# Kernel tuning notes

Hardware: AMD Instinct MI355X
Metric: run time of the kernel (lower is better)

The kernel has to match this reference:

```python
import jax, jax.numpy as jnp
import numpy as np

UFOLDS = 12
EPS = 1e-08


def _synapse_act(v, mu, sigma, W):
    # v: [B, P]; mu, sigma, W: [P, U] -> activation [B, P, U]
    g = jax.nn.sigmoid(sigma * (v[:, :, None] - mu))
    return W * g


def setup_inputs() -> dict:
    key = jax.random.key(0)
    ks = jax.random.split(key, 13)
    B, IN, U = 2048, 128, 256
    inputs = jax.random.normal(ks[0], (B, IN), dtype=jnp.float32)
    state = jax.random.normal(ks[1], (B, U), dtype=jnp.float32)
    # sensory synapse params (input_size, num_units)
    sensory_mu = jax.random.uniform(ks[2], (IN, U), minval=0.3, maxval=0.8)
    sensory_sigma = jax.random.uniform(ks[3], (IN, U), minval=3.0, maxval=8.0)
    sensory_W = jax.random.uniform(ks[4], (IN, U), minval=0.01, maxval=1.0)
    sensory_erev = jnp.sign(jax.random.normal(ks[5], (IN, U))).astype(jnp.float32)
    # recurrent synapse params (num_units, num_units)
    mu = jax.random.uniform(ks[6], (U, U), minval=0.3, maxval=0.8)
    sigma = jax.random.uniform(ks[7], (U, U), minval=3.0, maxval=8.0)
    W = jax.random.uniform(ks[8], (U, U), minval=0.01, maxval=1.0)
    erev = jnp.sign(jax.random.normal(ks[9], (U, U))).astype(jnp.float32)
    # leak / membrane params (num_units,)
    vleak = jax.random.uniform(ks[10], (U,), minval=-0.2, maxval=0.2)
    gleak = jnp.ones((U,), dtype=jnp.float32)          # gleak_init_min == gleak_init_max == 1
    cm_t = jnp.full((U,), 0.5, dtype=jnp.float32)      # cm_init_min == cm_init_max == 0.5
    return dict(inputs=inputs, state=state,
                sensory_mu=sensory_mu, sensory_sigma=sensory_sigma,
                sensory_W=sensory_W, sensory_erev=sensory_erev,
                mu=mu, sigma=sigma, W=W, erev=erev,
                vleak=vleak, gleak=gleak, cm_t=cm_t)


def reference(inputs, state, sensory_mu, sensory_sigma, sensory_W, sensory_erev,
              mu, sigma, W, erev, vleak, gleak, cm_t):
    # sensory path computed once, outside the fold loop
    s_act = _synapse_act(inputs, sensory_mu, sensory_sigma, sensory_W)  # [B, IN, U]
    w_den_sensory = jnp.sum(s_act, axis=1)                              # [B, U]
    w_num_sensory = jnp.sum(s_act * sensory_erev, axis=1)               # [B, U]

    gl_vl = gleak * vleak  # [U]

    def fold(v_pre, _):
        act = _synapse_act(v_pre, mu, sigma, W)           # [B, U, U]
        w_red = jnp.sum(act, axis=1)                       # [B, U]
        w_num = jnp.sum(act * erev, axis=1) + w_num_sensory
        numerator = cm_t * v_pre + gl_vl + w_num
        denominator = cm_t + gleak + w_red + w_den_sensory
        return numerator / (denominator + EPS), None

    v, _ = jax.lax.scan(fold, state, None, length=UFOLDS)
    return v
```

## Files before the change

kernel.cpp:

```cpp
#include <hip/hip_runtime.h>

#define NFOLDS 12
#define EPS 1e-8f
#define BATCH 2048
#define IN_DIM 128
#define UNITS 256
#define RB 4
#define LOG2E 1.44269504088896340736f

#if __has_builtin(__builtin_amdgcn_exp2f)
#define EXP2F(x) __builtin_amdgcn_exp2f(x)
#else
#define EXP2F(x) exp2f(x)
#endif

#if __has_builtin(__builtin_amdgcn_rcpf)
#define RCPF(x) __builtin_amdgcn_rcpf(x)
#else
#define RCPF(x) (1.0f / (x))
#endif

__global__ void prep_kernel(const float* __restrict__ mu,
                            const float* __restrict__ sigma,
                            const float* __restrict__ W,
                            const float* __restrict__ erev,
                            float4* __restrict__ out, int n) {
    int i = blockIdx.x * blockDim.x + threadIdx.x;
    if (i < n) {
        float A = sigma[i] * LOG2E;
        float w = W[i];
        out[i] = make_float4(-A, A * mu[i], w, w * erev[i]);
    }
}

__global__ __launch_bounds__(256, 2) void ltc_kernel(
    const float4* __restrict__ rp,
    const float4* __restrict__ sp,
    const float* __restrict__ inputs,
    const float* __restrict__ state,
    const float* __restrict__ vleak,
    const float* __restrict__ gleak,
    const float* __restrict__ cm_t,
    float* __restrict__ out)
{
    const int u = threadIdx.x;
    const int b0 = blockIdx.x * RB;

    __shared__ __align__(16) float v_sh[RB][UNITS];
    __shared__ float in_sh[RB][IN_DIM];

    #pragma unroll
    for (int rb = 0; rb < RB; ++rb)
        v_sh[rb][u] = state[(b0 + rb) * UNITS + u];
    #pragma unroll
    for (int k = u; k < RB * IN_DIM; k += UNITS) {
        int rb = k >> 7;
        int i  = k & (IN_DIM - 1);
        in_sh[rb][i] = inputs[(b0 + rb) * IN_DIM + i];
    }
    __syncthreads();

    float sden[RB], snum[RB];
    #pragma unroll
    for (int rb = 0; rb < RB; ++rb) { sden[rb] = 0.f; snum[rb] = 0.f; }

    for (int i = 0; i < IN_DIM; ++i) {
        float4 p = sp[i * UNITS + u];
        #pragma unroll
        for (int rb = 0; rb < RB; ++rb) {
            float t = fmaf(p.x, in_sh[rb][i], p.y);
            float e = EXP2F(t);
            float g = RCPF(1.0f + e);
            sden[rb] = fmaf(p.z, g, sden[rb]);
            snum[rb] = fmaf(p.w, g, snum[rb]);
        }
    }

    const float gl = gleak[u];
    const float cm = cm_t[u];
    const float glvl = gl * vleak[u];
    float den_base[RB], num_base[RB];
    #pragma unroll
    for (int rb = 0; rb < RB; ++rb) {
        den_base[rb] = cm + gl + sden[rb] + EPS;
        num_base[rb] = glvl + snum[rb];
    }

    float vnew[RB];
    for (int f = 0; f < NFOLDS; ++f) {
        float wred[RB], wnum[RB];
        #pragma unroll
        for (int rb = 0; rb < RB; ++rb) { wred[rb] = 0.f; wnum[rb] = 0.f; }

        for (int j = 0; j < UNITS; j += 4) {
            float4 p0 = rp[(j + 0) * UNITS + u];
            float4 p1 = rp[(j + 1) * UNITS + u];
            float4 p2 = rp[(j + 2) * UNITS + u];
            float4 p3 = rp[(j + 3) * UNITS + u];
            #pragma unroll
            for (int rb = 0; rb < RB; ++rb) {
                float4 v4 = *reinterpret_cast<const float4*>(&v_sh[rb][j]);
                {
                    float t = fmaf(p0.x, v4.x, p0.y);
                    float g = RCPF(1.0f + EXP2F(t));
                    wred[rb] = fmaf(p0.z, g, wred[rb]);
                    wnum[rb] = fmaf(p0.w, g, wnum[rb]);
                }
                {
                    float t = fmaf(p1.x, v4.y, p1.y);
                    float g = RCPF(1.0f + EXP2F(t));
                    wred[rb] = fmaf(p1.z, g, wred[rb]);
                    wnum[rb] = fmaf(p1.w, g, wnum[rb]);
                }
                {
                    float t = fmaf(p2.x, v4.z, p2.y);
                    float g = RCPF(1.0f + EXP2F(t));
                    wred[rb] = fmaf(p2.z, g, wred[rb]);
                    wnum[rb] = fmaf(p2.w, g, wnum[rb]);
                }
                {
                    float t = fmaf(p3.x, v4.w, p3.y);
                    float g = RCPF(1.0f + EXP2F(t));
                    wred[rb] = fmaf(p3.z, g, wred[rb]);
                    wnum[rb] = fmaf(p3.w, g, wnum[rb]);
                }
            }
        }

        #pragma unroll
        for (int rb = 0; rb < RB; ++rb) {
            float vp = v_sh[rb][u];
            float num = fmaf(cm, vp, num_base[rb]) + wnum[rb];
            float den = den_base[rb] + wred[rb];
            vnew[rb] = num / den;
        }
        __syncthreads();
        #pragma unroll
        for (int rb = 0; rb < RB; ++rb)
            v_sh[rb][u] = vnew[rb];
        __syncthreads();
    }

    #pragma unroll
    for (int rb = 0; rb < RB; ++rb)
        out[(b0 + rb) * UNITS + u] = vnew[rb];
}

extern "C" void kernel_launch(void* const* d_in, const int* in_sizes, int n_in,
                              void* d_out, int out_size, void* d_ws, size_t ws_size,
                              hipStream_t stream) {
    const float* inputs       = (const float*)d_in[0];
    const float* state        = (const float*)d_in[1];
    const float* sensory_mu   = (const float*)d_in[2];
    const float* sensory_sig  = (const float*)d_in[3];
    const float* sensory_W    = (const float*)d_in[4];
    const float* sensory_erev = (const float*)d_in[5];
    const float* mu           = (const float*)d_in[6];
    const float* sigma        = (const float*)d_in[7];
    const float* W            = (const float*)d_in[8];
    const float* erev         = (const float*)d_in[9];
    const float* vleak        = (const float*)d_in[10];
    const float* gleak        = (const float*)d_in[11];
    const float* cm_t         = (const float*)d_in[12];
    float* out = (float*)d_out;

    float4* rp = (float4*)d_ws;
    float4* sp = rp + UNITS * UNITS;

    int n_rec = UNITS * UNITS;
    int n_sen = IN_DIM * UNITS;
    prep_kernel<<<(n_rec + 255) / 256, 256, 0, stream>>>(mu, sigma, W, erev, rp, n_rec);
    prep_kernel<<<(n_sen + 255) / 256, 256, 0, stream>>>(sensory_mu, sensory_sig,
                                                         sensory_W, sensory_erev, sp, n_sen);

    ltc_kernel<<<BATCH / RB, UNITS, 0, stream>>>(rp, sp, inputs, state,
                                                 vleak, gleak, cm_t, out);
}
```

Before: 408.8 us.

## Split synapse reduction across two thread halves with shared-memory partial sums

Blocks grow from 256 to 512 threads. Each half sums over half of the presynaptic units (and half of the inputs in the sensory path), then the halves combine partial sums through shared memory. The goal is more waves per block and more latency hiding for the exp/rcp-heavy loop. The cost is an extra barrier per fold plus more shared-memory traffic, and the sensory loop now reads its inputs as vectorized float4.

```diff
diff --git a/kernel.cpp b/kernel.cpp
--- a/kernel.cpp
+++ b/kernel.cpp
@@ -33,7 +33,36 @@
     }
 }
 
-__global__ __launch_bounds__(256, 2) void ltc_kernel(
+__device__ __forceinline__ void syn4(const float4 p0, const float4 p1,
+                                     const float4 p2, const float4 p3,
+                                     const float4 v4, float& red, float& num) {
+    {
+        float t = fmaf(p0.x, v4.x, p0.y);
+        float g = RCPF(1.0f + EXP2F(t));
+        red = fmaf(p0.z, g, red);
+        num = fmaf(p0.w, g, num);
+    }
+    {
+        float t = fmaf(p1.x, v4.y, p1.y);
+        float g = RCPF(1.0f + EXP2F(t));
+        red = fmaf(p1.z, g, red);
+        num = fmaf(p1.w, g, num);
+    }
+    {
+        float t = fmaf(p2.x, v4.z, p2.y);
+        float g = RCPF(1.0f + EXP2F(t));
+        red = fmaf(p2.z, g, red);
+        num = fmaf(p2.w, g, num);
+    }
+    {
+        float t = fmaf(p3.x, v4.w, p3.y);
+        float g = RCPF(1.0f + EXP2F(t));
+        red = fmaf(p3.z, g, red);
+        num = fmaf(p3.w, g, num);
+    }
+}
+
+__global__ __launch_bounds__(512, 4) void ltc_kernel(
     const float4* __restrict__ rp,
     const float4* __restrict__ sp,
     const float* __restrict__ inputs,
@@ -43,56 +72,75 @@
     const float* __restrict__ cm_t,
     float* __restrict__ out)
 {
-    const int u = threadIdx.x;
+    const int tid = threadIdx.x;
+    const int u = tid & (UNITS - 1);
+    const int h = tid >> 8;
     const int b0 = blockIdx.x * RB;
 
     __shared__ __align__(16) float v_sh[RB][UNITS];
-    __shared__ float in_sh[RB][IN_DIM];
+    __shared__ __align__(16) float in_sh[RB][IN_DIM];
+    __shared__ float nb_sh[RB][UNITS];
+    __shared__ float db_sh[RB][UNITS];
+    __shared__ float cm_sh[UNITS];
+    __shared__ float pred[2][RB][UNITS];
+    __shared__ float pnum[2][RB][UNITS];
+
+    if (h == 0) {
+        #pragma unroll
+        for (int rb = 0; rb < RB; ++rb)
+            v_sh[rb][u] = state[(b0 + rb) * UNITS + u];
+        cm_sh[u] = cm_t[u];
+    } else {
+        #pragma unroll
+        for (int k = u; k < RB * IN_DIM; k += UNITS) {
+            int rb = k >> 7;
+            int i  = k & (IN_DIM - 1);
+            in_sh[rb][i] = inputs[(b0 + rb) * IN_DIM + i];
+        }
+    }
+    __syncthreads();
+
+    {
+        float sden[RB] = {0.f, 0.f, 0.f, 0.f};
+        float snum[RB] = {0.f, 0.f, 0.f, 0.f};
+        const int ibase = h * (IN_DIM / 2);
+        for (int ic = 0; ic < IN_DIM / 2; ic += 4) {
+            const int i = ibase + ic;
+            float4 p0 = sp[(i + 0) * UNITS + u];
+            float4 p1 = sp[(i + 1) * UNITS + u];
+            float4 p2 = sp[(i + 2) * UNITS + u];
+            float4 p3 = sp[(i + 3) * UNITS + u];
+            #pragma unroll
+            for (int rb = 0; rb < RB; ++rb) {
+                float4 x4 = *reinterpret_cast<const float4*>(&in_sh[rb][i]);
+                syn4(p0, p1, p2, p3, x4, sden[rb], snum[rb]);
+            }
+        }
+        #pragma unroll
+        for (int rb = 0; rb < RB; ++rb) {
+            pred[h][rb][u] = sden[rb];
+            pnum[h][rb][u] = snum[rb];
+        }
+    }
+    __syncthreads();
 
     #pragma unroll
-    for (int rb = 0; rb < RB; ++rb)
-        v_sh[rb][u] = state[(b0 + rb) * UNITS + u];
-    #pragma unroll
-    for (int k = u; k < RB * IN_DIM; k += UNITS) {
-        int rb = k >> 7;
-        int i  = k & (IN_DIM - 1);
-        in_sh[rb][i] = inputs[(b0 + rb) * IN_DIM + i];
+    for (int k = 0; k < 2; ++k) {
+        const int rb = h + 2 * k;
+        float gl = gleak[u];
+        float sd = pred[0][rb][u] + pred[1][rb][u];
+        float sn = pnum[0][rb][u] + pnum[1][rb][u];
+        db_sh[rb][u] = cm_sh[u] + gl + sd + EPS;
+        nb_sh[rb][u] = fmaf(gl, vleak[u], sn);
     }
     __syncthreads();
 
-    float sden[RB], snum[RB];
-    #pragma unroll
-    for (int rb = 0; rb < RB; ++rb) { sden[rb] = 0.f; snum[rb] = 0.f; }
-
-    for (int i = 0; i < IN_DIM; ++i) {
-        float4 p = sp[i * UNITS + u];
-        #pragma unroll
-        for (int rb = 0; rb < RB; ++rb) {
-            float t = fmaf(p.x, in_sh[rb][i], p.y);
-            float e = EXP2F(t);
-            float g = RCPF(1.0f + e);
-            sden[rb] = fmaf(p.z, g, sden[rb]);
-            snum[rb] = fmaf(p.w, g, snum[rb]);
-        }
-    }
-
-    const float gl = gleak[u];
-    const float cm = cm_t[u];
-    const float glvl = gl * vleak[u];
-    float den_base[RB], num_base[RB];
-    #pragma unroll
-    for (int rb = 0; rb < RB; ++rb) {
-        den_base[rb] = cm + gl + sden[rb] + EPS;
-        num_base[rb] = glvl + snum[rb];
-    }
-
-    float vnew[RB];
     for (int f = 0; f < NFOLDS; ++f) {
-        float wred[RB], wnum[RB];
-        #pragma unroll
-        for (int rb = 0; rb < RB; ++rb) { wred[rb] = 0.f; wnum[rb] = 0.f; }
-
-        for (int j = 0; j < UNITS; j += 4) {
+        float wred[RB] = {0.f, 0.f, 0.f, 0.f};
+        float wnum[RB] = {0.f, 0.f, 0.f, 0.f};
+        const int jbase = h * (UNITS / 2);
+        for (int jc = 0; jc < UNITS / 2; jc += 4) {
+            const int j = jbase + jc;
             float4 p0 = rp[(j + 0) * UNITS + u];
             float4 p1 = rp[(j + 1) * UNITS + u];
             float4 p2 = rp[(j + 2) * UNITS + u];
@@ -100,50 +148,31 @@
             #pragma unroll
             for (int rb = 0; rb < RB; ++rb) {
                 float4 v4 = *reinterpret_cast<const float4*>(&v_sh[rb][j]);
-                {
-                    float t = fmaf(p0.x, v4.x, p0.y);
-                    float g = RCPF(1.0f + EXP2F(t));
-                    wred[rb] = fmaf(p0.z, g, wred[rb]);
-                    wnum[rb] = fmaf(p0.w, g, wnum[rb]);
-                }
-                {
-                    float t = fmaf(p1.x, v4.y, p1.y);
-                    float g = RCPF(1.0f + EXP2F(t));
-                    wred[rb] = fmaf(p1.z, g, wred[rb]);
-                    wnum[rb] = fmaf(p1.w, g, wnum[rb]);
-                }
-                {
-                    float t = fmaf(p2.x, v4.z, p2.y);
-                    float g = RCPF(1.0f + EXP2F(t));
-                    wred[rb] = fmaf(p2.z, g, wred[rb]);
-                    wnum[rb] = fmaf(p2.w, g, wnum[rb]);
-                }
-                {
-                    float t = fmaf(p3.x, v4.w, p3.y);
-                    float g = RCPF(1.0f + EXP2F(t));
-                    wred[rb] = fmaf(p3.z, g, wred[rb]);
-                    wnum[rb] = fmaf(p3.w, g, wnum[rb]);
-                }
+                syn4(p0, p1, p2, p3, v4, wred[rb], wnum[rb]);
             }
         }
-
         #pragma unroll
         for (int rb = 0; rb < RB; ++rb) {
+            pred[h][rb][u] = wred[rb];
+            pnum[h][rb][u] = wnum[rb];
+        }
+        __syncthreads();
+
+        #pragma unroll
+        for (int k = 0; k < 2; ++k) {
+            const int rb = h + 2 * k;
+            float wr = pred[0][rb][u] + pred[1][rb][u];
+            float wn = pnum[0][rb][u] + pnum[1][rb][u];
             float vp = v_sh[rb][u];
-            float num = fmaf(cm, vp, num_base[rb]) + wnum[rb];
-            float den = den_base[rb] + wred[rb];
-            vnew[rb] = num / den;
+            float num = fmaf(cm_sh[u], vp, nb_sh[rb][u]) + wn;
+            float den = db_sh[rb][u] + wr;
+            float vn = num / den;
+            v_sh[rb][u] = vn;
+            if (f == NFOLDS - 1)
+                out[(b0 + rb) * UNITS + u] = vn;
         }
         __syncthreads();
-        #pragma unroll
-        for (int rb = 0; rb < RB; ++rb)
-            v_sh[rb][u] = vnew[rb];
-        __syncthreads();
-    }
-
-    #pragma unroll
-    for (int rb = 0; rb < RB; ++rb)
-        out[(b0 + rb) * UNITS + u] = vnew[rb];
+    }
 }
 
 extern "C" void kernel_launch(void* const* d_in, const int* in_sizes, int n_in,
@@ -173,6 +202,6 @@
     prep_kernel<<<(n_sen + 255) / 256, 256, 0, stream>>>(sensory_mu, sensory_sig,
                                                          sensory_W, sensory_erev, sp, n_sen);
 
-    ltc_kernel<<<BATCH / RB, UNITS, 0, stream>>>(rp, sp, inputs, state,
-                                                 vleak, gleak, cm_t, out);
-}
+    ltc_kernel<<<BATCH / RB, 512, 0, stream>>>(rp, sp, inputs, state,
+                                               vleak, gleak, cm_t, out);
+}
```

After: 385.9 us. 5.6% less time.
